# Optimization experiments

Hardware: AMD Instinct MI355X
Metric: run time of the kernel (lower is better)

## Reference

```python
import jax, jax.numpy as jnp
import numpy as np

B, H, D_OUT, T_STEPS = 256, 1024, 128, 128


def setup_inputs() -> dict:
    key = jax.random.key(0)
    ks = jax.random.split(key, 7)
    s = 1.0 / np.sqrt(H)
    return {
        "x": jax.random.normal(ks[0], (B, H), dtype=jnp.float32),
        "W_ih": jax.random.normal(ks[1], (4 * H, H), dtype=jnp.float32) * s,
        "W_hh": jax.random.normal(ks[2], (4 * H, H), dtype=jnp.float32) * s,
        "b_ih": jax.random.normal(ks[3], (4 * H,), dtype=jnp.float32) * s,
        "b_hh": jax.random.normal(ks[4], (4 * H,), dtype=jnp.float32) * s,
        "W_out": jax.random.normal(ks[5], (D_OUT, H), dtype=jnp.float32) * s,
        "b_out": jax.random.normal(ks[6], (D_OUT,), dtype=jnp.float32) * s,
        "T": T_STEPS,
    }


def reference(x, W_ih, W_hh, b_ih, b_hh, W_out, b_out, T):
    # first input is x. h0 = c0 = 0. PyTorch gate order: i, f, g, o.
    Hd = x.shape[1]
    b = b_ih + b_hh  # [4H]

    def step(carry, _):
        inp, h, c = carry  # each [B, H]
        gates = inp @ W_ih.T + h @ W_hh.T + b  # [B, 4H]
        i_g, f_g, g_g, o_g = jnp.split(gates, 4, axis=-1)
        c_new = jax.nn.sigmoid(f_g) * c + jax.nn.sigmoid(i_g) * jnp.tanh(g_g)
        h_new = jax.nn.sigmoid(o_g) * jnp.tanh(c_new)
        return (h_new, h_new, c_new), h_new

    zeros = jnp.zeros_like(x)
    _, seq = jax.lax.scan(step, (x, zeros, zeros), None, length=T)  # [T, B, H]
    out = seq @ W_out.T + b_out            # [T, B, D_out] (dropout is identity at eval)
    return jnp.transpose(out, (1, 0, 2))   # [B, T, D_out]
```

## Files before the change

### kernel.cpp

```cpp
#include <hip/hip_runtime.h>

typedef _Float16 half8 __attribute__((ext_vector_type(8)));
typedef _Float16 half4 __attribute__((ext_vector_type(4)));
typedef float    f32x4 __attribute__((ext_vector_type(4)));
typedef unsigned long long u64x2 __attribute__((ext_vector_type(2)));

constexpr int Bt   = 256;
constexpr int Hd   = 1024;
constexpr int G4   = 4096;
constexpr int Ts   = 128;
constexpr int DOUT = 128;

constexpr int NGROUP   = 8;
constexpr int WG_PER_G = 32;
constexpr int NWG      = NGROUP * WG_PER_G;
constexpr int NTHR     = 512;
constexpr int GROWS    = Bt / NGROUP;

constexpr size_t OFF_WSUM = 0;
constexpr size_t OFF_WIH  = OFF_WSUM + (size_t)G4 * Hd * 2;
constexpr size_t OFF_WOUT = OFF_WIH  + (size_t)G4 * Hd * 2;
constexpr size_t OFF_X    = OFF_WOUT + (size_t)DOUT * Hd * 2;
constexpr size_t OFF_BSUM = OFF_X    + (size_t)Bt * Hd * 2;
constexpr size_t OFF_BAR  = OFF_BSUM + (size_t)G4 * 4;
constexpr size_t OFF_SEQ  = OFF_BAR  + 4096;
constexpr size_t WS_NEED  = OFF_SEQ  + (size_t)Ts * Bt * Hd * 2;

__device__ __forceinline__ float fast_sig(float x) {
    return 1.f / (1.f + __expf(-x));
}
__device__ __forceinline__ float fast_tanh(float x) {
    float ax = fabsf(x);
    float e  = __expf(-2.f * ax);
    float t  = (1.f - e) / (1.f + e);
    return copysignf(t, x);
}

__device__ __forceinline__ void gload_lds16(const void* g, void* l) {
    __builtin_amdgcn_global_load_lds(
        (const __attribute__((address_space(1))) void*)g,
        (__attribute__((address_space(3))) void*)l, 16, 0, 0);
}

__device__ __forceinline__ void store16_wt(void* gp, u64x2 v) {
    asm volatile("global_store_dwordx4 %0, %1, off sc0 sc1"
                 :: "v"(gp), "v"(v) : "memory");
}
__device__ __forceinline__ void store4_wt(unsigned* gp, unsigned v) {
    asm volatile("global_store_dword %0, %1, off sc0 sc1"
                 :: "v"(gp), "v"(v) : "memory");
}
__device__ __forceinline__ unsigned load4_cp(const unsigned* gp) {
    unsigned v;
    asm volatile("global_load_dword %0, %1, off sc0 sc1\n\t"
                 "s_waitcnt vmcnt(0)"
                 : "=v"(v) : "v"(gp) : "memory");
    return v;
}

__global__ void prep_kernel(const float* __restrict__ Wih, const float* __restrict__ Whh,
                            const float* __restrict__ bih, const float* __restrict__ bhh,
                            const float* __restrict__ x,   const float* __restrict__ Wout,
                            _Float16* __restrict__ wsum16, _Float16* __restrict__ wih16,
                            _Float16* __restrict__ wout16, _Float16* __restrict__ x16,
                            float* __restrict__ bsum, unsigned* __restrict__ bar) {
    const int i0     = blockIdx.x * blockDim.x + threadIdx.x;
    const int stride = gridDim.x * blockDim.x;

    for (int i = i0; i < G4 * Hd / 4; i += stride) {
        f32x4 a = ((const f32x4*)Wih)[i];
        f32x4 b = ((const f32x4*)Whh)[i];
        half4 hs, hi;
        #pragma unroll
        for (int j = 0; j < 4; ++j) {
            hs[j] = (_Float16)(a[j] + b[j]);
            hi[j] = (_Float16)a[j];
        }
        ((half4*)wsum16)[i] = hs;
        ((half4*)wih16)[i]  = hi;
    }
    for (int i = i0; i < DOUT * Hd / 4; i += stride) {
        f32x4 a = ((const f32x4*)Wout)[i];
        half4 h;
        #pragma unroll
        for (int j = 0; j < 4; ++j) h[j] = (_Float16)a[j];
        ((half4*)wout16)[i] = h;
    }
    for (int i = i0; i < Bt * Hd / 4; i += stride) {
        f32x4 a = ((const f32x4*)x)[i];
        half4 h;
        #pragma unroll
        for (int j = 0; j < 4; ++j) h[j] = (_Float16)a[j];
        ((half4*)x16)[i] = h;
    }
    for (int i = i0; i < G4; i += stride) bsum[i] = bih[i] + bhh[i];
    for (int i = i0; i < 1024; i += stride)
        __hip_atomic_store(bar + i, 0u, __ATOMIC_RELAXED, __HIP_MEMORY_SCOPE_AGENT);
}

__launch_bounds__(NTHR, 2)
__global__ void lstm_kernel(const _Float16* __restrict__ wsum16,
                            const _Float16* __restrict__ wih16,
                            const _Float16* __restrict__ wout16,
                            const _Float16* __restrict__ x16,
                            const float* __restrict__ bsum,
                            const float* __restrict__ bout,
                            _Float16* __restrict__ seq,
                            float* __restrict__ out,
                            unsigned* __restrict__ bar) {
    __shared__ char smem[65536];

    const int bid = blockIdx.x;
    const int g   = bid & 7;
    const int wgi = bid >> 3;
    const int tid = threadIdx.x;
    const int wv  = tid >> 6;
    const int l   = tid & 63;
    const int lr  = l & 15;
    const int lk  = l >> 4;
    const int ks  = wv & 3;
    const int jg  = wv >> 2;
    const int j0  = wgi * 32 + jg * 16;
    const int brow0 = g * GROWS;

    unsigned* flags = bar + g * 64;

    float bias[4];
    #pragma unroll
    for (int gg = 0; gg < 4; ++gg) bias[gg] = bsum[gg * Hd + j0 + lr];

    half8 Bf[4][8];
    auto loadB = [&](const _Float16* __restrict__ W) {
        #pragma unroll
        for (int gg = 0; gg < 4; ++gg)
            #pragma unroll
            for (int kk = 0; kk < 8; ++kk)
                Bf[gg][kk] = *(const half8*)(W + (size_t)(gg * Hd + j0 + lr) * Hd
                                               + ks * 256 + kk * 32 + lk * 8);
    };

    auto stageA = [&](const _Float16* __restrict__ Asrc) {
        #pragma unroll
        for (int s = 0; s < 8; ++s) {
            const int i   = wv * 8 + s;
            const int row = i >> 1;
            const int bb  = (i & 1) * 64 + l;
            const int gb  = bb ^ (row & 7);
            gload_lds16((const char*)(Asrc + (size_t)row * Hd) + gb * 16,
                        smem + i * 1024);
        }
    };

    f32x4 c0 = {0.f,0.f,0.f,0.f}, c1 = {0.f,0.f,0.f,0.f};

    loadB(wih16);

    #pragma unroll 1
    for (int t = 0; t < Ts; ++t) {
        if (t > 0) {
            if (wv == 0) {
                const unsigned tgt = (unsigned)t;
                while (true) {
                    unsigned v = load4_cp(flags + (l & 31));
                    if (__all(v >= tgt)) break;
                    __builtin_amdgcn_s_sleep(1);
                }
            }
            __syncthreads();
        }

        const _Float16* Asrc = (t == 0)
            ? (x16 + (size_t)brow0 * Hd)
            : (seq + ((size_t)(t - 1) * Bt + brow0) * Hd);
        stageA(Asrc);
        __syncthreads();

        f32x4 acc[2][4];
        #pragma unroll
        for (int m = 0; m < 2; ++m)
            #pragma unroll
            for (int gg = 0; gg < 4; ++gg) acc[m][gg] = f32x4{0.f,0.f,0.f,0.f};

        #pragma unroll
        for (int kk = 0; kk < 8; ++kk) {
            half8 a[2];
            #pragma unroll
            for (int m = 0; m < 2; ++m) {
                const int row = m * 16 + lr;
                const int bb  = (ks * 32 + kk * 4 + lk) ^ (row & 7);
                a[m] = *(const half8*)(smem + row * 2048 + bb * 16);
            }
            #pragma unroll
            for (int gg = 0; gg < 4; ++gg) {
                acc[0][gg] = __builtin_amdgcn_mfma_f32_16x16x32_f16(a[0], Bf[gg][kk], acc[0][gg], 0,0,0);
                acc[1][gg] = __builtin_amdgcn_mfma_f32_16x16x32_f16(a[1], Bf[gg][kk], acc[1][gg], 0,0,0);
            }
        }
        __syncthreads();

        if (ks != 0) {
            float* dst = (float*)(smem + (size_t)(jg * 3 + (ks - 1)) * 8192);
            #pragma unroll
            for (int i = 0; i < 8; ++i)
                *(f32x4*)(dst + i * 256 + l * 4) = acc[i >> 2][i & 3];
        }
        __syncthreads();

        char* hst = smem + 49152;
        if (ks == 0) {
            #pragma unroll
            for (int s = 0; s < 3; ++s) {
                const float* src = (const float*)(smem + (size_t)(jg * 3 + s) * 8192);
                #pragma unroll
                for (int i = 0; i < 8; ++i)
                    acc[i >> 2][i & 3] += *(const f32x4*)(src + i * 256 + l * 4);
            }
            #pragma unroll
            for (int m = 0; m < 2; ++m) {
                f32x4& cc = m ? c1 : c0;
                #pragma unroll
                for (int r = 0; r < 4; ++r) {
                    float ig = fast_sig (acc[m][0][r] + bias[0]);
                    float fg = fast_sig (acc[m][1][r] + bias[1]);
                    float gv = fast_tanh(acc[m][2][r] + bias[2]);
                    float og = fast_sig (acc[m][3][r] + bias[3]);
                    float cn = fg * cc[r] + ig * gv;
                    cc[r] = cn;
                    float hv = og * fast_tanh(cn);
                    *(_Float16*)(hst + (m * 16 + lk * 4 + r) * 64 + (jg * 16 + lr) * 2)
                        = (_Float16)hv;
                }
            }
        }
        __syncthreads();

        if (wv == 0) {
            _Float16* hbase = seq + (size_t)t * Bt * Hd;
            #pragma unroll
            for (int s = 0; s < 2; ++s) {
                const int row = s * 16 + (l >> 2);
                const int q   = l & 3;
                u64x2 v = *(const u64x2*)(hst + row * 64 + q * 16);
                store16_wt(hbase + (size_t)(brow0 + row) * Hd + wgi * 32 + q * 8, v);
            }
            asm volatile("s_waitcnt vmcnt(0)" ::: "memory");
            if (l == 0) store4_wt(flags + wgi, (unsigned)(t + 1));
        }

        if (t == 0) loadB(wsum16);
    }

    if (wv == 0) {
        while (true) {
            unsigned v = load4_cp(flags + (l & 31));
            if (__all(v >= (unsigned)Ts)) break;
            __builtin_amdgcn_s_sleep(1);
        }
    }
    __syncthreads();

    {
        const int idx  = wgi * 8 + wv;
        const int t_   = idx >> 1;
        const int bb16 = brow0 + (idx & 1) * 16;
        const _Float16* abase = seq + ((size_t)t_ * Bt + bb16 + lr) * Hd + lk * 8;

        f32x4 oacc[8];
        #pragma unroll
        for (int ni = 0; ni < 8; ++ni) oacc[ni] = f32x4{0.f,0.f,0.f,0.f};

        #pragma unroll 2
        for (int k0 = 0; k0 < Hd; k0 += 32) {
            half8 a = *(const half8*)(abase + k0);
            #pragma unroll
            for (int ni = 0; ni < 8; ++ni) {
                half8 bf = *(const half8*)(wout16 + (size_t)(ni * 16 + lr) * Hd + lk * 8 + k0);
                oacc[ni] = __builtin_amdgcn_mfma_f32_16x16x32_f16(a, bf, oacc[ni], 0,0,0);
            }
        }
        #pragma unroll
        for (int ni = 0; ni < 8; ++ni) {
            const int d  = ni * 16 + lr;
            const float bo = bout[d];
            #pragma unroll
            for (int r = 0; r < 4; ++r) {
                const int b = bb16 + lk * 4 + r;
                out[(size_t)b * (Ts * DOUT) + t_ * DOUT + d] = oacc[ni][r] + bo;
            }
        }
    }
}

extern "C" void kernel_launch(void* const* d_in, const int* in_sizes, int n_in,
                              void* d_out, int out_size, void* d_ws, size_t ws_size,
                              hipStream_t stream) {
    const float* x    = (const float*)d_in[0];
    const float* Wih  = (const float*)d_in[1];
    const float* Whh  = (const float*)d_in[2];
    const float* bih  = (const float*)d_in[3];
    const float* bhh  = (const float*)d_in[4];
    const float* Wout = (const float*)d_in[5];
    const float* bout = (const float*)d_in[6];

    if (ws_size < WS_NEED) return;

    char* ws = (char*)d_ws;
    _Float16* wsum16 = (_Float16*)(ws + OFF_WSUM);
    _Float16* wih16  = (_Float16*)(ws + OFF_WIH);
    _Float16* wout16 = (_Float16*)(ws + OFF_WOUT);
    _Float16* x16    = (_Float16*)(ws + OFF_X);
    float*    bsum   = (float*)(ws + OFF_BSUM);
    unsigned* bar    = (unsigned*)(ws + OFF_BAR);
    _Float16* seq    = (_Float16*)(ws + OFF_SEQ);
    float*    outp   = (float*)d_out;

    hipLaunchKernelGGL(prep_kernel, dim3(1024), dim3(256), 0, stream,
                       Wih, Whh, bih, bhh, x, Wout,
                       wsum16, wih16, wout16, x16, bsum, bar);

    void* args[] = { &wsum16, &wih16, &wout16, &x16, &bsum,
                     (void*)&bout, &seq, &outp, &bar };
    hipLaunchCooperativeKernel((void*)lstm_kernel, dim3(NWG), dim3(NTHR),
                               args, 0, stream);
}
```

Before: 1.096 ms.

## Split batch group into two half-tiles and pipeline staging with compute via finer flags

Each workgroup now processes its 32 batch rows as two 16-row halves, double-buffering LDS so that staging one half's hidden state overlaps MFMA and the gate epilogue of the other half. Synchronisation moves to per-half, per-column-group flags so consumers wait only for the slice they need rather than the whole step. The hidden-state buffer is relaid out into 32-column blocks (blocked by producer workgroup) so each producer writes a contiguous chunk, and the x input and output projection are adapted to that layout. This trades extra barriers, more flag traffic and a more complex schedule for a shorter per-step critical path.

```diff
diff --git a/kernel.cpp b/kernel.cpp
--- a/kernel.cpp
+++ b/kernel.cpp
@@ -16,6 +16,8 @@
 constexpr int NWG      = NGROUP * WG_PER_G;
 constexpr int NTHR     = 512;
 constexpr int GROWS    = Bt / NGROUP;
+
+constexpr size_t SEQ_T = (size_t)32 * 256 * 64;
 
 constexpr size_t OFF_WSUM = 0;
 constexpr size_t OFF_WIH  = OFF_WSUM + (size_t)G4 * Hd * 2;
@@ -23,8 +25,8 @@
 constexpr size_t OFF_X    = OFF_WOUT + (size_t)DOUT * Hd * 2;
 constexpr size_t OFF_BSUM = OFF_X    + (size_t)Bt * Hd * 2;
 constexpr size_t OFF_BAR  = OFF_BSUM + (size_t)G4 * 4;
-constexpr size_t OFF_SEQ  = OFF_BAR  + 4096;
-constexpr size_t WS_NEED  = OFF_SEQ  + (size_t)Ts * Bt * Hd * 2;
+constexpr size_t OFF_SEQ  = OFF_BAR  + 131072;
+constexpr size_t WS_NEED  = OFF_SEQ  + (size_t)Ts * SEQ_T;
 
 __device__ __forceinline__ float fast_sig(float x) {
     return 1.f / (1.f + __expf(-x));
@@ -41,7 +43,6 @@
         (const __attribute__((address_space(1))) void*)g,
         (__attribute__((address_space(3))) void*)l, 16, 0, 0);
 }
-
 __device__ __forceinline__ void store16_wt(void* gp, u64x2 v) {
     asm volatile("global_store_dwordx4 %0, %1, off sc0 sc1"
                  :: "v"(gp), "v"(v) : "memory");
@@ -91,10 +92,14 @@
         half4 h;
         #pragma unroll
         for (int j = 0; j < 4; ++j) h[j] = (_Float16)a[j];
-        ((half4*)x16)[i] = h;
+        const int row = i >> 8;
+        const int e   = (i & 255) * 4;
+        const int jb  = e >> 5;
+        const int c   = e & 31;
+        ((half4*)x16)[(jb * 256 + row) * 8 + (c >> 2)] = h;
     }
     for (int i = i0; i < G4; i += stride) bsum[i] = bih[i] + bhh[i];
-    for (int i = i0; i < 1024; i += stride)
+    for (int i = i0; i < 32768; i += stride)
         __hip_atomic_store(bar + i, 0u, __ATOMIC_RELAXED, __HIP_MEMORY_SCOPE_AGENT);
 }
 
@@ -122,8 +127,9 @@
     const int jg  = wv >> 2;
     const int j0  = wgi * 32 + jg * 16;
     const int brow0 = g * GROWS;
-
-    unsigned* flags = bar + g * 64;
+    const bool lead = (ks == 0);
+
+    unsigned* gflags = bar + (size_t)g * 4096;
 
     float bias[4];
     #pragma unroll
@@ -139,121 +145,130 @@
                                                + ks * 256 + kk * 32 + lk * 8);
     };
 
-    auto stageA = [&](const _Float16* __restrict__ Asrc) {
-        #pragma unroll
-        for (int s = 0; s < 8; ++s) {
-            const int i   = wv * 8 + s;
+    const char* x16c = (const char*)x16;
+    char*       seqc = (char*)seq;
+
+    auto stageS = [&](char* Abase, const char* srcb, int rbase) {
+        #pragma unroll
+        for (int s = 0; s < 4; ++s) {
+            const int i   = wv * 4 + s;
             const int row = i >> 1;
-            const int bb  = (i & 1) * 64 + l;
-            const int gb  = bb ^ (row & 7);
-            gload_lds16((const char*)(Asrc + (size_t)row * Hd) + gb * 16,
-                        smem + i * 1024);
-        }
-    };
-
-    f32x4 c0 = {0.f,0.f,0.f,0.f}, c1 = {0.f,0.f,0.f,0.f};
+            const int gb  = ((i & 1) * 64 + l) ^ (row & 7);
+            const int jb  = gb >> 2;
+            const int q   = gb & 3;
+            gload_lds16(srcb + ((size_t)(jb * 256 + rbase + row)) * 64 + q * 16,
+                        Abase + i * 1024);
+        }
+    };
+
+    auto mfmaS = [&](char* Abase, f32x4* acc) {
+        #pragma unroll
+        for (int gg = 0; gg < 4; ++gg) acc[gg] = f32x4{0.f,0.f,0.f,0.f};
+        #pragma unroll
+        for (int kk = 0; kk < 8; ++kk) {
+            const int bb = (ks * 32 + kk * 4 + lk) ^ (lr & 7);
+            half8 a = *(const half8*)(Abase + lr * 2048 + bb * 16);
+            #pragma unroll
+            for (int gg = 0; gg < 4; ++gg)
+                acc[gg] = __builtin_amdgcn_mfma_f32_16x16x32_f16(a, Bf[gg][kk], acc[gg], 0,0,0);
+        }
+    };
+
+    auto dumpS = [&](char* Abase, const f32x4* acc) {
+        char* dst = Abase + (size_t)(jg * 3 + (ks - 1)) * 4096;
+        #pragma unroll
+        for (int gg = 0; gg < 4; ++gg)
+            *(f32x4*)(dst + gg * 1024 + l * 16) = acc[gg];
+    };
+
+    auto finishS = [&](char* Abase, f32x4* acc, f32x4& cc, int S, int t) {
+        #pragma unroll
+        for (int s = 0; s < 3; ++s) {
+            const char* src = Abase + (size_t)(jg * 3 + s) * 4096;
+            #pragma unroll
+            for (int gg = 0; gg < 4; ++gg)
+                acc[gg] += *(const f32x4*)(src + gg * 1024 + l * 16);
+        }
+        char* hst = Abase + 24576 + jg * 512;
+        #pragma unroll
+        for (int r = 0; r < 4; ++r) {
+            float ig = fast_sig (acc[0][r] + bias[0]);
+            float fg = fast_sig (acc[1][r] + bias[1]);
+            float gv = fast_tanh(acc[2][r] + bias[2]);
+            float og = fast_sig (acc[3][r] + bias[3]);
+            float cn = fg * cc[r] + ig * gv;
+            cc[r] = cn;
+            float hv = og * fast_tanh(cn);
+            *(_Float16*)(hst + (lk * 4 + r) * 32 + lr * 2) = (_Float16)hv;
+        }
+        if (l < 32) {
+            const int row = l >> 1;
+            const int q   = l & 1;
+            u64x2 v = *(const u64x2*)(hst + row * 32 + q * 16);
+            char* gp = seqc + (size_t)t * SEQ_T
+                     + ((size_t)(wgi * 256 + brow0 + S * 16 + row)) * 64
+                     + jg * 32 + q * 16;
+            store16_wt(gp, v);
+        }
+        asm volatile("s_waitcnt vmcnt(0)" ::: "memory");
+        if (l == 0)
+            store4_wt(gflags + wgi * 128 + S * 64 + jg * 32, (unsigned)(t + 1));
+    };
+
+    auto pollS = [&](int S, unsigned tgt) {
+        const unsigned* p = gflags + (l & 31) * 128 + S * 64 + (l >> 5) * 32;
+        while (true) {
+            unsigned v = load4_cp(p);
+            if (__all(v >= tgt)) break;
+            __builtin_amdgcn_s_sleep(1);
+        }
+    };
+
+    char* A_P = smem;
+    char* A_Q = smem + 32768;
+    f32x4 cP = {0.f,0.f,0.f,0.f}, cQ = {0.f,0.f,0.f,0.f};
+    f32x4 acc[4];
 
     loadB(wih16);
+
+    stageS(A_P, x16c, brow0);
+    __syncthreads();
 
     #pragma unroll 1
     for (int t = 0; t < Ts; ++t) {
-        if (t > 0) {
-            if (wv == 0) {
-                const unsigned tgt = (unsigned)t;
-                while (true) {
-                    unsigned v = load4_cp(flags + (l & 31));
-                    if (__all(v >= tgt)) break;
-                    __builtin_amdgcn_s_sleep(1);
-                }
-            }
+        const char* srcQ = (t == 0) ? x16c : (seqc + (size_t)(t - 1) * SEQ_T);
+
+        mfmaS(A_P, acc);
+        __syncthreads();
+        if (wv == 0) pollS(1, (unsigned)t);
+        else if (!lead) dumpS(A_P, acc);
+        __syncthreads();
+        stageS(A_Q, srcQ, brow0 + 16);
+        if (lead) finishS(A_P, acc, cP, 0, t);
+        __syncthreads();
+
+        mfmaS(A_Q, acc);
+        __syncthreads();
+        if (t < Ts - 1) {
+            if (wv == 0) pollS(0, (unsigned)(t + 1));
+            else if (!lead) dumpS(A_Q, acc);
             __syncthreads();
-        }
-
-        const _Float16* Asrc = (t == 0)
-            ? (x16 + (size_t)brow0 * Hd)
-            : (seq + ((size_t)(t - 1) * Bt + brow0) * Hd);
-        stageA(Asrc);
-        __syncthreads();
-
-        f32x4 acc[2][4];
-        #pragma unroll
-        for (int m = 0; m < 2; ++m)
-            #pragma unroll
-            for (int gg = 0; gg < 4; ++gg) acc[m][gg] = f32x4{0.f,0.f,0.f,0.f};
-
-        #pragma unroll
-        for (int kk = 0; kk < 8; ++kk) {
-            half8 a[2];
-            #pragma unroll
-            for (int m = 0; m < 2; ++m) {
-                const int row = m * 16 + lr;
-                const int bb  = (ks * 32 + kk * 4 + lk) ^ (row & 7);
-                a[m] = *(const half8*)(smem + row * 2048 + bb * 16);
-            }
-            #pragma unroll
-            for (int gg = 0; gg < 4; ++gg) {
-                acc[0][gg] = __builtin_amdgcn_mfma_f32_16x16x32_f16(a[0], Bf[gg][kk], acc[0][gg], 0,0,0);
-                acc[1][gg] = __builtin_amdgcn_mfma_f32_16x16x32_f16(a[1], Bf[gg][kk], acc[1][gg], 0,0,0);
-            }
-        }
-        __syncthreads();
-
-        if (ks != 0) {
-            float* dst = (float*)(smem + (size_t)(jg * 3 + (ks - 1)) * 8192);
-            #pragma unroll
-            for (int i = 0; i < 8; ++i)
-                *(f32x4*)(dst + i * 256 + l * 4) = acc[i >> 2][i & 3];
-        }
-        __syncthreads();
-
-        char* hst = smem + 49152;
-        if (ks == 0) {
-            #pragma unroll
-            for (int s = 0; s < 3; ++s) {
-                const float* src = (const float*)(smem + (size_t)(jg * 3 + s) * 8192);
-                #pragma unroll
-                for (int i = 0; i < 8; ++i)
-                    acc[i >> 2][i & 3] += *(const f32x4*)(src + i * 256 + l * 4);
-            }
-            #pragma unroll
-            for (int m = 0; m < 2; ++m) {
-                f32x4& cc = m ? c1 : c0;
-                #pragma unroll
-                for (int r = 0; r < 4; ++r) {
-                    float ig = fast_sig (acc[m][0][r] + bias[0]);
-                    float fg = fast_sig (acc[m][1][r] + bias[1]);
-                    float gv = fast_tanh(acc[m][2][r] + bias[2]);
-                    float og = fast_sig (acc[m][3][r] + bias[3]);
-                    float cn = fg * cc[r] + ig * gv;
-                    cc[r] = cn;
-                    float hv = og * fast_tanh(cn);
-                    *(_Float16*)(hst + (m * 16 + lk * 4 + r) * 64 + (jg * 16 + lr) * 2)
-                        = (_Float16)hv;
-                }
-            }
-        }
-        __syncthreads();
-
-        if (wv == 0) {
-            _Float16* hbase = seq + (size_t)t * Bt * Hd;
-            #pragma unroll
-            for (int s = 0; s < 2; ++s) {
-                const int row = s * 16 + (l >> 2);
-                const int q   = l & 3;
-                u64x2 v = *(const u64x2*)(hst + row * 64 + q * 16);
-                store16_wt(hbase + (size_t)(brow0 + row) * Hd + wgi * 32 + q * 8, v);
-            }
-            asm volatile("s_waitcnt vmcnt(0)" ::: "memory");
-            if (l == 0) store4_wt(flags + wgi, (unsigned)(t + 1));
-        }
-
+            stageS(A_P, seqc + (size_t)t * SEQ_T, brow0);
+        } else {
+            if (!lead) dumpS(A_Q, acc);
+            __syncthreads();
+        }
+        if (lead) finishS(A_Q, acc, cQ, 1, t);
         if (t == 0) loadB(wsum16);
+        __syncthreads();
     }
 
     if (wv == 0) {
+        const unsigned* p0 = gflags + (l & 31) * 128 + (l >> 5) * 32;
         while (true) {
-            unsigned v = load4_cp(flags + (l & 31));
-            if (__all(v >= (unsigned)Ts)) break;
+            unsigned a = load4_cp(p0);
+            unsigned b = load4_cp(p0 + 64);
+            if (__all((a >= (unsigned)Ts) & (b >= (unsigned)Ts))) break;
             __builtin_amdgcn_s_sleep(1);
         }
     }
@@ -263,7 +278,8 @@
         const int idx  = wgi * 8 + wv;
         const int t_   = idx >> 1;
         const int bb16 = brow0 + (idx & 1) * 16;
-        const _Float16* abase = seq + ((size_t)t_ * Bt + bb16 + lr) * Hd + lk * 8;
+        const int row  = bb16 + lr;
+        const char* ab = seqc + (size_t)t_ * SEQ_T + (size_t)row * 64 + lk * 16;
 
         f32x4 oacc[8];
         #pragma unroll
@@ -271,7 +287,7 @@
 
         #pragma unroll 2
         for (int k0 = 0; k0 < Hd; k0 += 32) {
-            half8 a = *(const half8*)(abase + k0);
+            half8 a = *(const half8*)(ab + (size_t)k0 * 512);
             #pragma unroll
             for (int ni = 0; ni < 8; ++ni) {
                 half8 bf = *(const half8*)(wout16 + (size_t)(ni * 16 + lr) * Hd + lk * 8 + k0);
```

Measured after the change: 985.5 us. 10.1% less time.
